# Optimization experiments

Hardware: AMD Instinct MI355X
Metric: run time of the kernel (lower is better)

The kernel has to match this reference:

```python
import jax, jax.numpy as jnp
import numpy as np

ALPHA = 0.2  # LeakyReLU negative slope
NEG_BIG = -9e15


def setup_inputs() -> dict:
    key = jax.random.key(0)
    k1, k2, k3, k4 = jax.random.split(key, 4)
    N, F_IN, F_OUT = 8192, 256, 64
    h = jax.random.normal(k1, (N, F_IN), dtype=jnp.float32)
    # binary dense adjacency (density ~0.5), kept as float32 as in the torch code
    adj = jax.random.randint(k2, (N, N), 0, 2).astype(jnp.float32)
    W = jax.random.normal(k3, (F_IN, F_OUT), dtype=jnp.float32) * 0.05
    a = jax.random.normal(k4, (2 * F_OUT, 1), dtype=jnp.float32) * 0.05
    return {"h": h, "adj": adj, "W": W, "a": a}


def reference(h, adj, W, a):
    F_OUT = W.shape[1]
    Wh = h @ W                               # [N, F]
    # Decomposed concat-attention score: e_ij = LeakyReLU(a1.Wh_i + a2.Wh_j)
    f_src = Wh @ a[:F_OUT, 0]                # [N]
    f_dst = Wh @ a[F_OUT:, 0]                # [N]
    e = f_src[:, None] + f_dst[None, :]      # [N, N]
    e = jnp.where(e > 0, e, ALPHA * e)       # LeakyReLU
    e = jnp.where(adj > 0, e, NEG_BIG)       # mask non-edges
    attention = jax.nn.softmax(e, axis=1)    # row softmax (dropout p=0 -> identity)
    h_prime = attention @ (adj @ Wh)         # note: double propagation as in source
    # concat=True -> ELU
    return jnp.where(h_prime > 0, h_prime, jnp.expm1(h_prime))
```

## Files before the change

### kernel.cpp

```cpp
#include <hip/hip_runtime.h>
#include <hip/hip_bf16.h>


#define N 8192

typedef float f32x4 __attribute__((ext_vector_type(4)));
typedef short s16x8 __attribute__((ext_vector_type(8)));
typedef unsigned long long u64;
typedef u64 u64x2 __attribute__((ext_vector_type(2)));

union PF { s16x8 v; unsigned u[4]; };

__device__ __forceinline__ unsigned short f2bf(float x) {
  unsigned u = __float_as_uint(x);
  u += 0x7FFFu + ((u >> 16) & 1u);
  return (unsigned short)(u >> 16);
}
__device__ __forceinline__ unsigned pack2(unsigned short lo, unsigned short hi) {
  return (unsigned)lo | ((unsigned)hi << 16);
}
__device__ __forceinline__ unsigned packrn(float lo, float hi) {
  return ((__float_as_uint(lo) + 0x8000u) >> 16) |
         ((__float_as_uint(hi) + 0x8000u) & 0xFFFF0000u);
}

#define MFMA __builtin_amdgcn_mfma_f32_16x16x32_bf16

__global__ __launch_bounds__(256) void kA(const float* __restrict__ adj,
                                          const float* __restrict__ h,
                                          const float* __restrict__ W,
                                          const float* __restrict__ a,
                                          u64* __restrict__ ML,
                                          unsigned short* __restrict__ Bpack,
                                          float* __restrict__ expg,
                                          float* __restrict__ expg2,
                                          float* __restrict__ Af,
                                          float* __restrict__ Cf,
                                          float* __restrict__ Enf) {
  const int l = threadIdx.x & 63;
  const int w = threadIdx.x >> 6;
  const int i = (blockIdx.x << 1) + (w & 1);
  if (w < 2) {
    const float* ap = adj + (size_t)i * N + (l << 2);
    u64* mp = ML + (size_t)i * 128;
    f32x4 v0 = *(const f32x4*)(ap);
    f32x4 v1 = *(const f32x4*)(ap + 256);
    f32x4 v2 = *(const f32x4*)(ap + 512);
    f32x4 v3 = *(const f32x4*)(ap + 768);
    for (int cc = 0; cc < 32; cc += 4) {
      const int cn = (cc < 28) ? (cc + 4) : cc;
      f32x4 n0 = *(const f32x4*)(ap + ((cn + 0) << 8));
      f32x4 n1 = *(const f32x4*)(ap + ((cn + 1) << 8));
      f32x4 n2 = *(const f32x4*)(ap + ((cn + 2) << 8));
      f32x4 n3 = *(const f32x4*)(ap + ((cn + 3) << 8));
      u64 b0  = __ballot(v0.x > 0.f), b1  = __ballot(v0.y > 0.f);
      u64 b2  = __ballot(v0.z > 0.f), b3  = __ballot(v0.w > 0.f);
      u64 b4  = __ballot(v1.x > 0.f), b5  = __ballot(v1.y > 0.f);
      u64 b6  = __ballot(v1.z > 0.f), b7  = __ballot(v1.w > 0.f);
      u64 b8  = __ballot(v2.x > 0.f), b9  = __ballot(v2.y > 0.f);
      u64 b10 = __ballot(v2.z > 0.f), b11 = __ballot(v2.w > 0.f);
      u64 b12 = __ballot(v3.x > 0.f), b13 = __ballot(v3.y > 0.f);
      u64 b14 = __ballot(v3.z > 0.f), b15 = __ballot(v3.w > 0.f);
      if (l == 0) {
        u64x2* q = (u64x2*)(mp + (cc << 2));
        u64x2 t0; t0.x = b0;  t0.y = b1;  q[0] = t0;
        u64x2 t1; t1.x = b2;  t1.y = b3;  q[1] = t1;
        u64x2 t2; t2.x = b4;  t2.y = b5;  q[2] = t2;
        u64x2 t3; t3.x = b6;  t3.y = b7;  q[3] = t3;
        u64x2 t4; t4.x = b8;  t4.y = b9;  q[4] = t4;
        u64x2 t5; t5.x = b10; t5.y = b11; q[5] = t5;
        u64x2 t6; t6.x = b12; t6.y = b13; q[6] = t6;
        u64x2 t7; t7.x = b14; t7.y = b15; q[7] = t7;
      }
      v0 = n0; v1 = n1; v2 = n2; v3 = n3;
    }
  } else {
    const float* hrow = h + (size_t)i * 256;
    float acc = 0.f;
#pragma unroll 4
    for (int kb = 0; kb < 64; ++kb) {
      f32x4 hv = *(const f32x4*)(hrow + (kb << 2));
      acc += hv.x * W[((kb << 2) + 0) * 64 + l];
      acc += hv.y * W[((kb << 2) + 1) * 64 + l];
      acc += hv.z * W[((kb << 2) + 2) * 64 + l];
      acc += hv.w * W[((kb << 2) + 3) * 64 + l];
    }
    float s1 = acc * a[l];
    float s2 = acc * a[64 + l];
#pragma unroll
    for (int d = 32; d > 0; d >>= 1) {
      s1 += __shfl_xor(s1, d);
      s2 += __shfl_xor(s2, d);
    }
    if (l == 0) {
      expg[i]  = __expf(s2);
      expg2[i] = __expf(0.2f * s2);
      Af[i]    = __expf(s1);
      Cf[i]    = __expf(0.2f * s1);
      Enf[i]   = __expf(-s1);
    }
    const int kb = i >> 5;
    const int b = l >> 4;
    const int lp = (l & 15) | (((i >> 3) & 3) << 4);
    const int e = i & 7;
    Bpack[(((size_t)(kb * 4 + b)) * 64 + lp) * 8 + e] = f2bf(acc);
  }
}

__global__ __launch_bounds__(512) void k2b(const u64* __restrict__ ML,
                                           const unsigned short* __restrict__ Bpack,
                                           unsigned short* __restrict__ Upack) {
  __shared__ float red[2][8][64][16];
  const int l = threadIdx.x & 63;
  const int w = threadIdx.x >> 6;
  const int i0 = blockIdx.x << 5;
  const int r = l & 15, kg = l >> 4;
  const s16x8* Bv = (const s16x8*)Bpack;
  const u64x2* mrow0 = (const u64x2*)(ML + (size_t)(i0 + r) * 128);
  const u64x2* mrow1 = (const u64x2*)(ML + (size_t)(i0 + 16 + r) * 128);
  const int sh0 = kg << 1;
  f32x4 x0 = {0.f,0.f,0.f,0.f}, x1 = x0, x2 = x0, x3 = x0;
  f32x4 y0 = x0, y1 = x0, y2 = x0, y3 = x0;
  const int jb0 = w << 5;
  s16x8 c0, c1, c2, c3;
  {
    const size_t bi = ((size_t)jb0 << 8) + l;
    c0 = Bv[bi]; c1 = Bv[bi + 64]; c2 = Bv[bi + 128]; c3 = Bv[bi + 192];
  }
  for (int cc = 0; cc < 4; ++cc) {
    const int c = (w << 2) + cc;
    u64x2 ma = mrow0[(c << 1)], mb = mrow0[(c << 1) + 1];
    const u64 xa0 = ma.x >> sh0, xa1 = ma.y >> sh0,
              xa2 = mb.x >> sh0, xa3 = mb.y >> sh0;
    u64x2 mc = mrow1[(c << 1)], md = mrow1[(c << 1) + 1];
    const u64 ya0 = mc.x >> sh0, ya1 = mc.y >> sh0,
              ya2 = md.x >> sh0, ya3 = md.y >> sh0;
#pragma unroll
    for (int j7 = 0; j7 < 8; ++j7) {
      const int jb = (c << 3) + j7;
      const int jbn = (cc == 3 && j7 == 7) ? jb : (jb + 1);
      const size_t bn = ((size_t)jbn << 8) + l;
      s16x8 n0 = Bv[bn], n1 = Bv[bn + 64], n2 = Bv[bn + 128], n3 = Bv[bn + 192];
      const unsigned p0 = (unsigned)(xa0 >> (j7 << 3)) & 1u;
      const unsigned p1 = (unsigned)(xa1 >> (j7 << 3)) & 1u;
      const unsigned p2 = (unsigned)(xa2 >> (j7 << 3)) & 1u;
      const unsigned p3 = (unsigned)(xa3 >> (j7 << 3)) & 1u;
      const unsigned p4 = (unsigned)(xa0 >> ((j7 << 3) + 1)) & 1u;
      const unsigned p5 = (unsigned)(xa1 >> ((j7 << 3) + 1)) & 1u;
      const unsigned p6 = (unsigned)(xa2 >> ((j7 << 3) + 1)) & 1u;
      const unsigned p7 = (unsigned)(xa3 >> ((j7 << 3) + 1)) & 1u;
      const unsigned q0 = (unsigned)(ya0 >> (j7 << 3)) & 1u;
      const unsigned q1 = (unsigned)(ya1 >> (j7 << 3)) & 1u;
      const unsigned q2 = (unsigned)(ya2 >> (j7 << 3)) & 1u;
      const unsigned q3 = (unsigned)(ya3 >> (j7 << 3)) & 1u;
      const unsigned q4 = (unsigned)(ya0 >> ((j7 << 3) + 1)) & 1u;
      const unsigned q5 = (unsigned)(ya1 >> ((j7 << 3) + 1)) & 1u;
      const unsigned q6 = (unsigned)(ya2 >> ((j7 << 3) + 1)) & 1u;
      const unsigned q7 = (unsigned)(ya3 >> ((j7 << 3) + 1)) & 1u;
      s16x8 af0, af1;
      af0[0] = p0 ? (short)0x3F80 : (short)0;
      af0[1] = p1 ? (short)0x3F80 : (short)0;
      af0[2] = p2 ? (short)0x3F80 : (short)0;
      af0[3] = p3 ? (short)0x3F80 : (short)0;
      af0[4] = p4 ? (short)0x3F80 : (short)0;
      af0[5] = p5 ? (short)0x3F80 : (short)0;
      af0[6] = p6 ? (short)0x3F80 : (short)0;
      af0[7] = p7 ? (short)0x3F80 : (short)0;
      af1[0] = q0 ? (short)0x3F80 : (short)0;
      af1[1] = q1 ? (short)0x3F80 : (short)0;
      af1[2] = q2 ? (short)0x3F80 : (short)0;
      af1[3] = q3 ? (short)0x3F80 : (short)0;
      af1[4] = q4 ? (short)0x3F80 : (short)0;
      af1[5] = q5 ? (short)0x3F80 : (short)0;
      af1[6] = q6 ? (short)0x3F80 : (short)0;
      af1[7] = q7 ? (short)0x3F80 : (short)0;
      x0 = MFMA(af0, c0, x0, 0, 0, 0);
      x1 = MFMA(af0, c1, x1, 0, 0, 0);
      x2 = MFMA(af0, c2, x2, 0, 0, 0);
      x3 = MFMA(af0, c3, x3, 0, 0, 0);
      y0 = MFMA(af1, c0, y0, 0, 0, 0);
      y1 = MFMA(af1, c1, y1, 0, 0, 0);
      y2 = MFMA(af1, c2, y2, 0, 0, 0);
      y3 = MFMA(af1, c3, y3, 0, 0, 0);
      c0 = n0; c1 = n1; c2 = n2; c3 = n3;
    }
  }
#pragma unroll
  for (int q = 0; q < 4; ++q) {
    red[0][w][l][q] = x0[q]; red[0][w][l][4 + q] = x1[q];
    red[0][w][l][8 + q] = x2[q]; red[0][w][l][12 + q] = x3[q];
    red[1][w][l][q] = y0[q]; red[1][w][l][4 + q] = y1[q];
    red[1][w][l][8 + q] = y2[q]; red[1][w][l][12 + q] = y3[q];
  }
  __syncthreads();
  const int tl = threadIdx.x & 63;
  const int b = (threadIdx.x >> 6) & 3;
  const int sE = threadIdx.x >> 8;
  const int reg0 = sE << 1;
#pragma unroll
  for (int s = 0; s < 2; ++s) {
    float u0 = 0.f, u1 = 0.f;
#pragma unroll
    for (int w8 = 0; w8 < 8; ++w8) {
      u0 += red[s][w8][tl][(b << 2) + reg0];
      u1 += red[s][w8][tl][(b << 2) + reg0 + 1];
    }
    const int k0 = i0 + (s << 4) + ((tl >> 4) << 2) + reg0;
    const unsigned pkv = pack2(f2bf(u0), f2bf(u1));
    const int kbD = k0 >> 5, lgrp = (k0 >> 3) & 3, e0 = k0 & 7;
    *(unsigned*)((char*)Upack +
        ((size_t)((kbD << 2) + b) * 64 + ((tl & 15) | (lgrp << 4))) * 16 + (e0 << 1)) = pkv;
  }
}

__global__ __launch_bounds__(512) void k3(const u64* __restrict__ ML,
                                          const unsigned short* __restrict__ Upack,
                                          const float* __restrict__ expg,
                                          const float* __restrict__ expg2,
                                          const float* __restrict__ Af,
                                          const float* __restrict__ Cf,
                                          const float* __restrict__ Enf,
                                          float* __restrict__ out) {
  __shared__ float red[2][8][64][16];
  __shared__ float wred[2][8][16];
  const int l = threadIdx.x & 63;
  const int w = threadIdx.x >> 6;
  const int i0 = blockIdx.x << 5;
  const int r = l & 15, kg = l >> 4;
  const float enf0 = Enf[i0 + r],      enf1 = Enf[i0 + 16 + r];
  const float Ar0 = Af[i0 + r],        Cr0 = Cf[i0 + r];
  const float Ar1 = Af[i0 + 16 + r],   Cr1 = Cf[i0 + 16 + r];
  const s16x8* Uv = (const s16x8*)Upack;
  const u64x2* mrow0 = (const u64x2*)(ML + (size_t)(i0 + r) * 128);
  const u64x2* mrow1 = (const u64x2*)(ML + (size_t)(i0 + 16 + r) * 128);
  const int sh0 = kg << 1;
  const s16x8 ones = {(short)0x3F80, (short)0x3F80, (short)0x3F80, (short)0x3F80,
                      (short)0x3F80, (short)0x3F80, (short)0x3F80, (short)0x3F80};
  f32x4 x0 = {0.f,0.f,0.f,0.f}, x1 = x0, x2 = x0, x3 = x0, xd = x0;
  f32x4 y0 = x0, y1 = x0, y2 = x0, y3 = x0, yd = x0;
  const int jb0 = w << 5;
  s16x8 c0, c1, c2, c3;
  {
    const size_t bi = ((size_t)jb0 << 8) + l;
    c0 = Uv[bi]; c1 = Uv[bi + 64]; c2 = Uv[bi + 128]; c3 = Uv[bi + 192];
  }
  for (int cc = 0; cc < 4; ++cc) {
    const int c = (w << 2) + cc;
    u64x2 ma = mrow0[(c << 1)], mb = mrow0[(c << 1) + 1];
    const u64 xa0 = ma.x >> sh0, xa1 = ma.y >> sh0,
              xa2 = mb.x >> sh0, xa3 = mb.y >> sh0;
    u64x2 mc = mrow1[(c << 1)], md = mrow1[(c << 1) + 1];
    const u64 ya0 = mc.x >> sh0, ya1 = mc.y >> sh0,
              ya2 = md.x >> sh0, ya3 = md.y >> sh0;
#pragma unroll
    for (int j7 = 0; j7 < 8; ++j7) {
      const int jb = (c << 3) + j7;
      const int jbn = (cc == 3 && j7 == 7) ? jb : (jb + 1);
      const size_t bn = ((size_t)jbn << 8) + l;
      s16x8 n0 = Uv[bn], n1 = Uv[bn + 64], n2 = Uv[bn + 128], n3 = Uv[bn + 192];
      f32x4 eg0 = *(const f32x4*)(expg + (jb << 5) + (kg << 3));
      f32x4 eg1 = *(const f32x4*)(expg + (jb << 5) + (kg << 3) + 4);
      f32x4 eh0 = *(const f32x4*)(expg2 + (jb << 5) + (kg << 3));
      f32x4 eh1 = *(const f32x4*)(expg2 + (jb << 5) + (kg << 3) + 4);
#define WT(wq, sh, egv, ehv, enf, Ar, Cr)                                    \
      ((((wq) >> (sh)) & 1ull) ?                                             \
        (((egv) > (enf)) ? (Ar) * (egv) : (Cr) * (ehv)) : 0.f)
      const float w00 = WT(xa0, (j7 << 3),     eg0.x, eh0.x, enf0, Ar0, Cr0);
      const float w01 = WT(xa1, (j7 << 3),     eg0.y, eh0.y, enf0, Ar0, Cr0);
      const float w02 = WT(xa2, (j7 << 3),     eg0.z, eh0.z, enf0, Ar0, Cr0);
      const float w03 = WT(xa3, (j7 << 3),     eg0.w, eh0.w, enf0, Ar0, Cr0);
      const float w04 = WT(xa0, (j7 << 3) + 1, eg1.x, eh1.x, enf0, Ar0, Cr0);
      const float w05 = WT(xa1, (j7 << 3) + 1, eg1.y, eh1.y, enf0, Ar0, Cr0);
      const float w06 = WT(xa2, (j7 << 3) + 1, eg1.z, eh1.z, enf0, Ar0, Cr0);
      const float w07 = WT(xa3, (j7 << 3) + 1, eg1.w, eh1.w, enf0, Ar0, Cr0);
      const float w10 = WT(ya0, (j7 << 3),     eg0.x, eh0.x, enf1, Ar1, Cr1);
      const float w11 = WT(ya1, (j7 << 3),     eg0.y, eh0.y, enf1, Ar1, Cr1);
      const float w12 = WT(ya2, (j7 << 3),     eg0.z, eh0.z, enf1, Ar1, Cr1);
      const float w13 = WT(ya3, (j7 << 3),     eg0.w, eh0.w, enf1, Ar1, Cr1);
      const float w14 = WT(ya0, (j7 << 3) + 1, eg1.x, eh1.x, enf1, Ar1, Cr1);
      const float w15 = WT(ya1, (j7 << 3) + 1, eg1.y, eh1.y, enf1, Ar1, Cr1);
      const float w16 = WT(ya2, (j7 << 3) + 1, eg1.z, eh1.z, enf1, Ar1, Cr1);
      const float w17 = WT(ya3, (j7 << 3) + 1, eg1.w, eh1.w, enf1, Ar1, Cr1);
#undef WT
      PF pf0, pf1;
      pf0.u[0] = packrn(w00, w01); pf0.u[1] = packrn(w02, w03);
      pf0.u[2] = packrn(w04, w05); pf0.u[3] = packrn(w06, w07);
      pf1.u[0] = packrn(w10, w11); pf1.u[1] = packrn(w12, w13);
      pf1.u[2] = packrn(w14, w15); pf1.u[3] = packrn(w16, w17);
      x0 = MFMA(pf0.v, c0, x0, 0, 0, 0);
      x1 = MFMA(pf0.v, c1, x1, 0, 0, 0);
      x2 = MFMA(pf0.v, c2, x2, 0, 0, 0);
      x3 = MFMA(pf0.v, c3, x3, 0, 0, 0);
      xd = MFMA(pf0.v, ones, xd, 0, 0, 0);
      y0 = MFMA(pf1.v, c0, y0, 0, 0, 0);
      y1 = MFMA(pf1.v, c1, y1, 0, 0, 0);
      y2 = MFMA(pf1.v, c2, y2, 0, 0, 0);
      y3 = MFMA(pf1.v, c3, y3, 0, 0, 0);
      yd = MFMA(pf1.v, ones, yd, 0, 0, 0);
      c0 = n0; c1 = n1; c2 = n2; c3 = n3;
    }
  }
  if (r == 0) {
#pragma unroll
    for (int q = 0; q < 4; ++q) {
      wred[0][w][(kg << 2) + q] = xd[q];
      wred[1][w][(kg << 2) + q] = yd[q];
    }
  }
#pragma unroll
  for (int q = 0; q < 4; ++q) {
    red[0][w][l][q] = x0[q]; red[0][w][l][4 + q] = x1[q];
    red[0][w][l][8 + q] = x2[q]; red[0][w][l][12 + q] = x3[q];
    red[1][w][l][q] = y0[q]; red[1][w][l][4 + q] = y1[q];
    red[1][w][l][8 + q] = y2[q]; red[1][w][l][12 + q] = y3[q];
  }
  __syncthreads();
  const int tl = threadIdx.x & 63;
  const int b = (threadIdx.x >> 6) & 3;
  const int sE = threadIdx.x >> 8;
#pragma unroll
  for (int s = 0; s < 2; ++s) {
#pragma unroll
    for (int q = 0; q < 2; ++q) {
      const int reg = (sE << 1) + q;
      const int idx = (b << 2) + reg;
      const int row = ((tl >> 4) << 2) + reg;
      float sv = 0.f, dv = 0.f;
#pragma unroll
      for (int w8 = 0; w8 < 8; ++w8) {
        sv += red[s][w8][tl][idx];
        dv += wred[s][w8][row];
      }
      dv = (dv > 0.f) ? dv : 1.f;
      float v = sv / dv;
      v = (v > 0.f) ? v : (__expf(v) - 1.f);
      out[(size_t)(i0 + (s << 4) + row) * 64 + (b << 4) + (tl & 15)] = v;
    }
  }
}

extern "C" void kernel_launch(void* const* d_in, const int* in_sizes, int n_in,
                              void* d_out, int out_size, void* d_ws, size_t ws_size,
                              hipStream_t stream) {
  const float* h   = (const float*)d_in[0];
  const float* adj = (const float*)d_in[1];
  const float* W   = (const float*)d_in[2];
  const float* a   = (const float*)d_in[3];
  float* out = (float*)d_out;
  char* ws = (char*)d_ws;
  unsigned short* Bpack = (unsigned short*)(ws);
  unsigned short* Upack = (unsigned short*)(ws + (1u << 20));
  float* expg  = (float*)(ws + (2u << 20));
  float* expg2 = (float*)(ws + (2u << 20) + 1u * 32768u);
  float* Af    = (float*)(ws + (2u << 20) + 2u * 32768u);
  float* Cf    = (float*)(ws + (2u << 20) + 3u * 32768u);
  float* Enf   = (float*)(ws + (2u << 20) + 4u * 32768u);
  u64* ML = (u64*)(ws + (3u << 20));

  hipLaunchKernelGGL(kA,  dim3(4096), dim3(256), 0, stream,
                     adj, h, W, a, ML, Bpack, expg, expg2, Af, Cf, Enf);
  hipLaunchKernelGGL(k2b, dim3(256), dim3(512), 0, stream,
                     ML, Bpack, Upack);
  hipLaunchKernelGGL(k3,  dim3(256), dim3(512), 0, stream,
                     ML, Upack, expg, expg2, Af, Cf, Enf, out);
}
```

Before: 133.5 us.

## Split adjacency bitmask and Wh projection into separate blocks with more loads in flight

Kernel kA now gives each adjacency row its own 256-thread block, with all four waves loading eight float4 chunks each up front. The ballots are collected in shared memory and written out once per row. The h@W projection moves to separate trailing blocks, four rows per block, so the grid grows to 10240 blocks. The aim is more memory-level parallelism on the 256MB adjacency read, which dominates the kernel. The cost is an extra LDS round trip and a block-wide sync per row.

```diff
diff --git a/kernel.cpp b/kernel.cpp
--- a/kernel.cpp
+++ b/kernel.cpp
@@ -37,44 +37,42 @@
                                           float* __restrict__ Af,
                                           float* __restrict__ Cf,
                                           float* __restrict__ Enf) {
+  __shared__ u64 mbuf[128];
   const int l = threadIdx.x & 63;
   const int w = threadIdx.x >> 6;
-  const int i = (blockIdx.x << 1) + (w & 1);
-  if (w < 2) {
-    const float* ap = adj + (size_t)i * N + (l << 2);
-    u64* mp = ML + (size_t)i * 128;
-    f32x4 v0 = *(const f32x4*)(ap);
-    f32x4 v1 = *(const f32x4*)(ap + 256);
-    f32x4 v2 = *(const f32x4*)(ap + 512);
-    f32x4 v3 = *(const f32x4*)(ap + 768);
-    for (int cc = 0; cc < 32; cc += 4) {
-      const int cn = (cc < 28) ? (cc + 4) : cc;
-      f32x4 n0 = *(const f32x4*)(ap + ((cn + 0) << 8));
-      f32x4 n1 = *(const f32x4*)(ap + ((cn + 1) << 8));
-      f32x4 n2 = *(const f32x4*)(ap + ((cn + 2) << 8));
-      f32x4 n3 = *(const f32x4*)(ap + ((cn + 3) << 8));
-      u64 b0  = __ballot(v0.x > 0.f), b1  = __ballot(v0.y > 0.f);
-      u64 b2  = __ballot(v0.z > 0.f), b3  = __ballot(v0.w > 0.f);
-      u64 b4  = __ballot(v1.x > 0.f), b5  = __ballot(v1.y > 0.f);
-      u64 b6  = __ballot(v1.z > 0.f), b7  = __ballot(v1.w > 0.f);
-      u64 b8  = __ballot(v2.x > 0.f), b9  = __ballot(v2.y > 0.f);
-      u64 b10 = __ballot(v2.z > 0.f), b11 = __ballot(v2.w > 0.f);
-      u64 b12 = __ballot(v3.x > 0.f), b13 = __ballot(v3.y > 0.f);
-      u64 b14 = __ballot(v3.z > 0.f), b15 = __ballot(v3.w > 0.f);
-      if (l == 0) {
-        u64x2* q = (u64x2*)(mp + (cc << 2));
-        u64x2 t0; t0.x = b0;  t0.y = b1;  q[0] = t0;
-        u64x2 t1; t1.x = b2;  t1.y = b3;  q[1] = t1;
-        u64x2 t2; t2.x = b4;  t2.y = b5;  q[2] = t2;
-        u64x2 t3; t3.x = b6;  t3.y = b7;  q[3] = t3;
-        u64x2 t4; t4.x = b8;  t4.y = b9;  q[4] = t4;
-        u64x2 t5; t5.x = b10; t5.y = b11; q[5] = t5;
-        u64x2 t6; t6.x = b12; t6.y = b13; q[6] = t6;
-        u64x2 t7; t7.x = b14; t7.y = b15; q[7] = t7;
-      }
-      v0 = n0; v1 = n1; v2 = n2; v3 = n3;
+  const int bid = blockIdx.x;
+  if (bid < 8192) {
+    const int i = bid;
+    const float* ap = adj + (size_t)i * N + (w << 11) + (l << 2);
+    f32x4 v0 = *(const f32x4*)(ap + (0 << 8));
+    f32x4 v1 = *(const f32x4*)(ap + (1 << 8));
+    f32x4 v2 = *(const f32x4*)(ap + (2 << 8));
+    f32x4 v3 = *(const f32x4*)(ap + (3 << 8));
+    f32x4 v4 = *(const f32x4*)(ap + (4 << 8));
+    f32x4 v5 = *(const f32x4*)(ap + (5 << 8));
+    f32x4 v6 = *(const f32x4*)(ap + (6 << 8));
+    f32x4 v7 = *(const f32x4*)(ap + (7 << 8));
+#define KCH(vk, c) {                                                      \
+    u64 B0 = __ballot(vk.x > 0.f);                                        \
+    u64 B1 = __ballot(vk.y > 0.f);                                        \
+    u64 B2 = __ballot(vk.z > 0.f);                                        \
+    u64 B3 = __ballot(vk.w > 0.f);                                        \
+    if (l == 0) {                                                         \
+      u64x2* q = (u64x2*)&mbuf[(w << 5) + ((c) << 2)];                    \
+      u64x2 t0; t0.x = B0; t0.y = B1;                                     \
+      u64x2 t1; t1.x = B2; t1.y = B3;                                     \
+      q[0] = t0; q[1] = t1;                                               \
+    } }
+    KCH(v0, 0) KCH(v1, 1) KCH(v2, 2) KCH(v3, 3)
+    KCH(v4, 4) KCH(v5, 5) KCH(v6, 6) KCH(v7, 7)
+#undef KCH
+    __syncthreads();
+    if (w == 0) {
+      u64x2 mv = *((const u64x2*)&mbuf[l << 1]);
+      ((u64x2*)(ML + (size_t)i * 128))[l] = mv;
     }
   } else {
+    const int i = ((bid - 8192) << 2) + w;
     const float* hrow = h + (size_t)i * 256;
     float acc = 0.f;
 #pragma unroll 4
@@ -357,7 +355,7 @@
   float* Enf   = (float*)(ws + (2u << 20) + 4u * 32768u);
   u64* ML = (u64*)(ws + (3u << 20));
 
-  hipLaunchKernelGGL(kA,  dim3(4096), dim3(256), 0, stream,
+  hipLaunchKernelGGL(kA,  dim3(10240), dim3(256), 0, stream,
                      adj, h, W, a, ML, Bpack, expg, expg2, Af, Cf, Enf);
   hipLaunchKernelGGL(k2b, dim3(256), dim3(512), 0, stream,
                      ML, Bpack, Upack);
```

Result: slower. 138.4 us (+3.6%).
